# Kernel tuning notes

Measured on AMD Instinct MI355X. Metric: run time of the kernel, lower is better.

## Reference

```python
import jax, jax.numpy as jnp
import numpy as np

LEVELS = [5023, 1256, 314, 79, 20]  # mesh vertex counts, fine -> coarse
T = 64        # number of audio frames
LATENT = 128  # latent_channels
S = 9         # spiral length
OUT_CH = [32, 64, 64, 128]


def setup_inputs() -> dict:
    key = jax.random.key(0)
    ks = list(jax.random.split(key, 40))
    nk = lambda: ks.pop()
    inp = {}
    inp["latent"] = jax.random.normal(nk(), (T, LATENT), jnp.float32)
    inp["actor"] = jax.random.normal(nk(), (LEVELS[0], 3), jnp.float32)
    # spiral indices per mesh level (levels 0..3 carry SpiralConvs)
    for l in range(4):
        n = LEVELS[l]
        inp[f"spiral{l}"] = jax.random.randint(nk(), (n, S), 0, n)
    # sparse up-transforms: level l+1 (coarse) -> level l (fine), ~3 nnz per fine vertex
    for l in range(4):
        nf, nc = LEVELS[l], LEVELS[l + 1]
        nnz = 3 * nf
        inp[f"up{l}_rows"] = jax.random.randint(nk(), (nnz,), 0, nf)
        inp[f"up{l}_cols"] = jax.random.randint(nk(), (nnz,), 0, nc)
        inp[f"up{l}_vals"] = jax.random.uniform(nk(), (nnz,), jnp.float32)
    def lin(k, od, idim):
        scale = np.sqrt(2.0 / (od + idim)).astype(np.float32)  # xavier-uniform-ish std
        return jax.random.normal(k, (od, idim), jnp.float32) * scale
    # de_layers[0]: Linear(latent -> num_vert * out_channels[-1])
    inp["W0"] = lin(nk(), LEVELS[4] * OUT_CH[-1], LATENT)
    inp["b0"] = jnp.zeros((LEVELS[4] * OUT_CH[-1],), jnp.float32)
    # SpiralDeblock convs (coarse -> fine): 128->128, 128->64, 64->64, 64->32
    inp["W1"] = lin(nk(), 128, 128 * S); inp["b1"] = jnp.zeros((128,), jnp.float32)
    inp["W2"] = lin(nk(), 64, 128 * S);  inp["b2"] = jnp.zeros((64,), jnp.float32)
    inp["W3"] = lin(nk(), 64, 64 * S);   inp["b3"] = jnp.zeros((64,), jnp.float32)
    inp["W4"] = lin(nk(), 32, 64 * S);   inp["b4"] = jnp.zeros((32,), jnp.float32)
    # final SpiralConv 32 -> 3 (init=True in torch zeros it; use small randn for testing)
    inp["Wf"] = lin(nk(), 3, 32 * S) * 0.1
    inp["bf"] = jnp.zeros((3,), jnp.float32)
    return inp


def spiral_conv(x, idx, W, b):
    # x: [T, n_in, C]; idx: [n, S] -> gather spiral neighborhoods, flatten, linear
    t, n = x.shape[0], idx.shape[0]
    g = x[:, idx.reshape(-1), :].reshape(t, n, -1)  # [T, n, S*C]
    return g @ W.T + b


def pool(x, rows, cols, vals, n_out):
    # sparse up-transform: out[:, rows] += x[:, cols] * vals  (scatter-add)
    g = x[:, cols, :] * vals[None, :, None]  # [T, nnz, C]
    return jnp.zeros((x.shape[0], n_out, x.shape[2]), x.dtype).at[:, rows].add(g)


def reference(latent, actor, spiral0, spiral1, spiral2, spiral3,
              up0_rows, up0_cols, up0_vals, up1_rows, up1_cols, up1_vals,
              up2_rows, up2_cols, up2_vals, up3_rows, up3_cols, up3_vals,
              W0, b0, W1, b1, W2, b2, W3, b3, W4, b4, Wf, bf):
    t = latent.shape[0]
    x = (latent @ W0.T + b0).reshape(t, LEVELS[4], OUT_CH[-1])  # [T, 20, 128]
    x = jax.nn.elu(spiral_conv(pool(x, up3_rows, up3_cols, up3_vals, LEVELS[3]), spiral3, W1, b1))
    x = jax.nn.elu(spiral_conv(pool(x, up2_rows, up2_cols, up2_vals, LEVELS[2]), spiral2, W2, b2))
    x = jax.nn.elu(spiral_conv(pool(x, up1_rows, up1_cols, up1_vals, LEVELS[1]), spiral1, W3, b3))
    x = jax.nn.elu(spiral_conv(pool(x, up0_rows, up0_cols, up0_vals, LEVELS[0]), spiral0, W4, b4))
    x = spiral_conv(x, spiral0, Wf, bf)  # [T, 5023, 3]
    return x + actor[None]  # per-frame offsets added to neutral actor mesh
```

## Files before the change

kernel.cpp:

```cpp
#include <hip/hip_runtime.h>
#include <hip/hip_bf16.h>

#define T_FRAMES 64

typedef __bf16 bf16x8 __attribute__((ext_vector_type(8)));
typedef float f32x4 __attribute__((ext_vector_type(4)));

#define NNZ0 15069
#define NNZ1 3768
#define NNZ2 942
#define NNZ3 237
#define N0 5023
#define N1 1256
#define N2 314
#define N3 79
#define N4 20


__global__ __launch_bounds__(256) void linear0_kernel(
    const float* __restrict__ latent, const float* __restrict__ W0,
    const float* __restrict__ b0, __bf16* __restrict__ out) {
  int id = blockIdx.x * 256 + threadIdx.x;
  if (id >= 64 * 2560) return;
  int j = id % 2560;
  int t = id / 2560;
  const float* lrow = latent + t * 128;
  const float* wrow = W0 + j * 128;
  float acc = b0[j];
#pragma unroll 8
  for (int k = 0; k < 128; ++k) acc = fmaf(lrow[k], wrow[k], acc);
  out[((size_t)(j >> 7) * 64 + t) * 128 + (j & 127)] = (__bf16)acc;
}

__global__ __launch_bounds__(256) void cvt_all_kernel(
    const float* __restrict__ W1, const float* __restrict__ W2,
    const float* __restrict__ W3, const float* __restrict__ W4,
    const float* __restrict__ Wf, __bf16* __restrict__ o) {
  int i = blockIdx.x * 256 + threadIdx.x;
  if (i < 147456) { o[i] = (__bf16)W1[i]; return; }
  if (i < 221184) { o[i] = (__bf16)W2[i - 147456]; return; }
  if (i < 258048) { o[i] = (__bf16)W3[i - 221184]; return; }
  if (i < 276480) { o[i] = (__bf16)W4[i - 258048]; return; }
  if (i < 281088) {
    int j = i - 276480;
    o[i] = (j / 288 < 3) ? (__bf16)Wf[j] : (__bf16)0.f;
  }
}

__global__ __launch_bounds__(256) void csr_count_kernel(
    const int* __restrict__ r0, const int* __restrict__ r1,
    const int* __restrict__ r2, const int* __restrict__ r3,
    int* __restrict__ c0, int* __restrict__ c1,
    int* __restrict__ c2, int* __restrict__ c3) {
  int i = blockIdx.x * 256 + threadIdx.x;
  if (i < NNZ0) atomicAdd(&c0[r0[i]], 1);
  else if (i < NNZ0 + NNZ1) atomicAdd(&c1[r1[i - NNZ0]], 1);
  else if (i < NNZ0 + NNZ1 + NNZ2) atomicAdd(&c2[r2[i - NNZ0 - NNZ1]], 1);
  else if (i < NNZ0 + NNZ1 + NNZ2 + NNZ3) atomicAdd(&c3[r3[i - NNZ0 - NNZ1 - NNZ2]], 1);
}

__global__ __launch_bounds__(256) void csr_scan_kernel(
    const int* __restrict__ c0, const int* __restrict__ c1,
    const int* __restrict__ c2, const int* __restrict__ c3,
    int* __restrict__ o0, int* __restrict__ o1,
    int* __restrict__ o2, int* __restrict__ o3,
    int* __restrict__ u0, int* __restrict__ u1,
    int* __restrict__ u2, int* __restrict__ u3) {
  const int b = blockIdx.x;
  const int* counts = b == 0 ? c0 : b == 1 ? c1 : b == 2 ? c2 : c3;
  int* off = b == 0 ? o0 : b == 1 ? o1 : b == 2 ? o2 : o3;
  int* cur = b == 0 ? u0 : b == 1 ? u1 : b == 2 ? u2 : u3;
  const int n = b == 0 ? N0 : b == 1 ? N1 : b == 2 ? N2 : N3;

  __shared__ int part[256];
  const int chunk = (n + 255) / 256;
  const int start = threadIdx.x * chunk;
  const int end = min(start + chunk, n);
  int s = 0;
  for (int i = start; i < end; ++i) s += counts[i];
  part[threadIdx.x] = s;
  __syncthreads();
  for (int d = 1; d < 256; d <<= 1) {
    int v = (threadIdx.x >= d) ? part[threadIdx.x - d] : 0;
    __syncthreads();
    part[threadIdx.x] += v;
    __syncthreads();
  }
  int run = (threadIdx.x == 0) ? 0 : part[threadIdx.x - 1];
  for (int i = start; i < end; ++i) {
    off[i] = run;
    cur[i] = run;
    run += counts[i];
  }
  if (threadIdx.x == 255) off[n] = run;
}

__global__ __launch_bounds__(256) void csr_bucket_kernel(
    const int* __restrict__ r0, const int* __restrict__ r1,
    const int* __restrict__ r2, const int* __restrict__ r3,
    const int* __restrict__ q0, const int* __restrict__ q1,
    const int* __restrict__ q2, const int* __restrict__ q3,
    const float* __restrict__ v0, const float* __restrict__ v1,
    const float* __restrict__ v2, const float* __restrict__ v3,
    int* __restrict__ u0, int* __restrict__ u1,
    int* __restrict__ u2, int* __restrict__ u3,
    int2* __restrict__ p0, int2* __restrict__ p1,
    int2* __restrict__ p2, int2* __restrict__ p3) {
  int i = blockIdx.x * 256 + threadIdx.x;
  if (i < NNZ0) {
    int p = atomicAdd(&u0[r0[i]], 1);
    p0[p] = make_int2(q0[i], __float_as_int(v0[i]));
  } else if (i < NNZ0 + NNZ1) {
    int e = i - NNZ0;
    int p = atomicAdd(&u1[r1[e]], 1);
    p1[p] = make_int2(q1[e], __float_as_int(v1[e]));
  } else if (i < NNZ0 + NNZ1 + NNZ2) {
    int e = i - NNZ0 - NNZ1;
    int p = atomicAdd(&u2[r2[e]], 1);
    p2[p] = make_int2(q2[e], __float_as_int(v2[e]));
  } else if (i < NNZ0 + NNZ1 + NNZ2 + NNZ3) {
    int e = i - NNZ0 - NNZ1 - NNZ2;
    int p = atomicAdd(&u3[r3[e]], 1);
    p3[p] = make_int2(q3[e], __float_as_int(v3[e]));
  }
}

template <int C, int TT>
__global__ __launch_bounds__(256) void pool_csr_kernel(
    const __bf16* __restrict__ x, const int* __restrict__ off,
    const int2* __restrict__ pk, __bf16* __restrict__ out, int n_out) {
  unsigned id = blockIdx.x * 256u + threadIdx.x;
  unsigned total = (unsigned)n_out * (T_FRAMES / TT) * C;
  if (id >= total) return;
  const int c = id % C;
  const unsigned rt = id / C;
  const int tb = rt % (T_FRAMES / TT);
  const int row = rt / (T_FRAMES / TT);

  const int o0 = off[row], o1 = off[row + 1];
  float acc[TT];
#pragma unroll
  for (int u = 0; u < TT; ++u) acc[u] = 0.f;

  for (int j = o0; j < o1; ++j) {
    const int2 rec = pk[j];
    const float val = __int_as_float(rec.y);
    const __bf16* xp = x + ((size_t)rec.x * T_FRAMES + tb * TT) * C + c;
#pragma unroll
    for (int u = 0; u < TT; ++u)
      acc[u] = fmaf(val, (float)xp[(size_t)u * C], acc[u]);
  }

  __bf16* op = out + ((size_t)row * T_FRAMES + tb * TT) * C + c;
#pragma unroll
  for (int u = 0; u < TT; ++u) op[(size_t)u * C] = (__bf16)acc[u];
}

template <int CIN, int COUT, int WV, int MT>
__global__ __launch_bounds__(256) void conv_mfma_kernel(
    const __bf16* __restrict__ x, const int* __restrict__ idx,
    const __bf16* __restrict__ Wb, const float* __restrict__ bias,
    __bf16* __restrict__ out) {
  constexpr int K = 9 * CIN;
  constexpr int KK = K / 32;
  constexpr int NT = COUT / 16;

  const int lane = threadIdx.x & 63;
  const int wid = threadIdx.x >> 6;
  const int v = blockIdx.x;
  const int tq0 = (blockIdx.y * WV + wid) * MT;
  const int col = lane & 15;
  const int kg = lane >> 4;

  size_t vbase[9];
#pragma unroll
  for (int s = 0; s < 9; ++s)
    vbase[s] = (size_t)idx[v * 9 + s] * (T_FRAMES * CIN);

  bf16x8 a[MT][KK];
#pragma unroll
  for (int mt = 0; mt < MT; ++mt) {
    const size_t trow = (size_t)(tq0 + mt) * 16 + col;
#pragma unroll
    for (int kk = 0; kk < KK; ++kk) {
      const int s = (kk * 32) / CIN;
      const int ci0 = (kk * 32) % CIN;
      a[mt][kk] = *(const bf16x8*)(x + vbase[s] + trow * CIN + ci0 + kg * 8);
    }
  }

  f32x4 acc[MT][NT];
#pragma unroll
  for (int nt = 0; nt < NT; ++nt) {
    float b = bias[nt * 16 + col];
#pragma unroll
    for (int mt = 0; mt < MT; ++mt) acc[mt][nt] = (f32x4){b, b, b, b};
  }

#pragma unroll
  for (int kk = 0; kk < KK; ++kk) {
#pragma unroll
    for (int nt = 0; nt < NT; ++nt) {
      bf16x8 bfr = *(const bf16x8*)(Wb + (size_t)(nt * 16 + col) * K + kk * 32 + kg * 8);
#pragma unroll
      for (int mt = 0; mt < MT; ++mt)
        acc[mt][nt] = __builtin_amdgcn_mfma_f32_16x16x32_bf16(a[mt][kk], bfr, acc[mt][nt], 0, 0, 0);
    }
  }

#pragma unroll
  for (int mt = 0; mt < MT; ++mt) {
#pragma unroll
    for (int j = 0; j < 4; ++j) {
      const size_t tr = (size_t)(tq0 + mt) * 16 + kg * 4 + j;
#pragma unroll
      for (int nt = 0; nt < NT; ++nt) {
        float aa = acc[mt][nt][j];
        aa = aa > 0.f ? aa : expm1f(aa);
        out[((size_t)v * T_FRAMES + tr) * COUT + nt * 16 + col] = (__bf16)aa;
      }
    }
  }
}

__global__ __launch_bounds__(256) void final_mfma_kernel(
    const __bf16* __restrict__ x, const int* __restrict__ idx,
    const __bf16* __restrict__ Wfp, const float* __restrict__ bf3,
    const float* __restrict__ actor, float* __restrict__ out) {
  const int lane = threadIdx.x & 63;
  const int wid = threadIdx.x >> 6;
  const int v = blockIdx.x;
  const int col = lane & 15;
  const int kg = lane >> 4;
  const size_t trow = (size_t)wid * 16 + col;

  bf16x8 a[9];
#pragma unroll
  for (int s = 0; s < 9; ++s)
    a[s] = *(const bf16x8*)(x + (size_t)idx[v * 9 + s] * (T_FRAMES * 32) + trow * 32 + kg * 8);

  float b = (col < 3) ? bf3[col] : 0.f;
  f32x4 acc = (f32x4){b, b, b, b};

#pragma unroll
  for (int kk = 0; kk < 9; ++kk) {
    bf16x8 w = *(const bf16x8*)(Wfp + col * 288 + kk * 32 + kg * 8);
    acc = __builtin_amdgcn_mfma_f32_16x16x32_bf16(a[kk], w, acc, 0, 0, 0);
  }

  if (col < 3) {
    const float av = actor[v * 3 + col];
#pragma unroll
    for (int j = 0; j < 4; ++j) {
      const int tr = wid * 16 + kg * 4 + j;
      out[((size_t)tr * N0 + v) * 3 + col] = acc[j] + av;
    }
  }
}

extern "C" void kernel_launch(void* const* d_in, const int* in_sizes, int n_in_args,
                              void* d_out, int out_size, void* d_ws, size_t ws_size,
                              hipStream_t stream) {
  const float* latent = (const float*)d_in[0];
  const float* actor  = (const float*)d_in[1];
  const int* spiral0 = (const int*)d_in[2];
  const int* spiral1 = (const int*)d_in[3];
  const int* spiral2 = (const int*)d_in[4];
  const int* spiral3 = (const int*)d_in[5];
  const int* up0_rows = (const int*)d_in[6];
  const int* up0_cols = (const int*)d_in[7];
  const float* up0_vals = (const float*)d_in[8];
  const int* up1_rows = (const int*)d_in[9];
  const int* up1_cols = (const int*)d_in[10];
  const float* up1_vals = (const float*)d_in[11];
  const int* up2_rows = (const int*)d_in[12];
  const int* up2_cols = (const int*)d_in[13];
  const float* up2_vals = (const float*)d_in[14];
  const int* up3_rows = (const int*)d_in[15];
  const int* up3_cols = (const int*)d_in[16];
  const float* up3_vals = (const float*)d_in[17];
  const float* W0 = (const float*)d_in[18];
  const float* b0 = (const float*)d_in[19];
  const float* W1 = (const float*)d_in[20];
  const float* b1 = (const float*)d_in[21];
  const float* W2 = (const float*)d_in[22];
  const float* b2 = (const float*)d_in[23];
  const float* W3 = (const float*)d_in[24];
  const float* b3 = (const float*)d_in[25];
  const float* W4 = (const float*)d_in[26];
  const float* b4 = (const float*)d_in[27];
  const float* Wf = (const float*)d_in[28];
  const float* bf3 = (const float*)d_in[29];
  float* out = (float*)d_out;

  __bf16* poolbuf = (__bf16*)d_ws;
  __bf16* convout = poolbuf + 20574208;
  __bf16* wbuf = convout + 10287104;
  __bf16* W1b = wbuf;
  __bf16* W2b = W1b + 147456;
  __bf16* W3b = W2b + 73728;
  __bf16* W4b = W3b + 36864;
  __bf16* Wfp = W4b + 18432;
  int* csr = (int*)(wbuf + 281088);
  int* cnt0 = csr;            int* cnt1 = cnt0 + N0;   int* cnt2 = cnt1 + N1;   int* cnt3 = cnt2 + N2;
  int* off0 = csr + 6672;     int* off1 = off0 + N0+1; int* off2 = off1 + N1+1; int* off3 = off2 + N2+1;
  int* cur0 = csr + 13348;    int* cur1 = cur0 + N0;   int* cur2 = cur1 + N1;   int* cur3 = cur2 + N2;
  int2* pk0 = (int2*)(csr + 20020);
  int2* pk1 = pk0 + NNZ0;
  int2* pk2 = pk1 + NNZ1;
  int2* pk3 = pk2 + NNZ2;

  hipMemsetAsync(cnt0, 0, 6672 * sizeof(int), stream);
  csr_count_kernel<<<(20016 + 255) / 256, 256, 0, stream>>>(
      up0_rows, up1_rows, up2_rows, up3_rows, cnt0, cnt1, cnt2, cnt3);
  csr_scan_kernel<<<4, 256, 0, stream>>>(cnt0, cnt1, cnt2, cnt3,
                                         off0, off1, off2, off3,
                                         cur0, cur1, cur2, cur3);
  csr_bucket_kernel<<<(20016 + 255) / 256, 256, 0, stream>>>(
      up0_rows, up1_rows, up2_rows, up3_rows,
      up0_cols, up1_cols, up2_cols, up3_cols,
      up0_vals, up1_vals, up2_vals, up3_vals,
      cur0, cur1, cur2, cur3, pk0, pk1, pk2, pk3);

  cvt_all_kernel<<<(281088 + 255) / 256, 256, 0, stream>>>(W1, W2, W3, W4, Wf, wbuf);

  linear0_kernel<<<(64 * 2560 + 255) / 256, 256, 0, stream>>>(latent, W0, b0, convout);

  pool_csr_kernel<128, 16><<<(N3 * 4 * 128 + 255) / 256, 256, 0, stream>>>(
      convout, off3, pk3, poolbuf, N3);
  conv_mfma_kernel<128, 128, 1, 1><<<dim3(N3, 4), 64, 0, stream>>>(
      poolbuf, spiral3, W1b, b1, convout);

  pool_csr_kernel<128, 16><<<(N2 * 4 * 128 + 255) / 256, 256, 0, stream>>>(
      convout, off2, pk2, poolbuf, N2);
  conv_mfma_kernel<128, 64, 1, 1><<<dim3(N2, 4), 64, 0, stream>>>(
      poolbuf, spiral2, W2b, b2, convout);

  pool_csr_kernel<64, 16><<<(N1 * 4 * 64 + 255) / 256, 256, 0, stream>>>(
      convout, off1, pk1, poolbuf, N1);
  conv_mfma_kernel<64, 64, 2, 2><<<dim3(N1, 1), 128, 0, stream>>>(
      poolbuf, spiral1, W3b, b3, convout);

  pool_csr_kernel<64, 16><<<(N0 * 4 * 64 + 255) / 256, 256, 0, stream>>>(
      convout, off0, pk0, poolbuf, N0);
  conv_mfma_kernel<64, 32, 2, 2><<<dim3(N0, 1), 128, 0, stream>>>(
      poolbuf, spiral0, W4b, b4, convout);

  final_mfma_kernel<<<N0, 256, 0, stream>>>(convout, spiral0, Wfp, bf3, actor, out);
}
```

Baseline: 406.2 us.

## Reorder final spiral conv: project per vertex first, then gather-sum projections

Splits the final 32->3 spiral convolution into a dense per-vertex MFMA projection against each of the 9 spiral weight slices, followed by a gather kernel that sums the projected 3-channel values over spiral neighbours and adds bias and actor. This cuts the gathered data per output vertex from 32 channels to 4. In exchange it adds a kernel launch, a temporary buffer written and re-read, and bf16 rounding of partial sums. Launch bounds for the conv kernel are also tightened to match the actual block size.

```diff
diff --git a/kernel.cpp b/kernel.cpp
--- a/kernel.cpp
+++ b/kernel.cpp
@@ -4,6 +4,7 @@
 #define T_FRAMES 64
 
 typedef __bf16 bf16x8 __attribute__((ext_vector_type(8)));
+typedef __bf16 bf16x4 __attribute__((ext_vector_type(4)));
 typedef float f32x4 __attribute__((ext_vector_type(4)));
 
 #define NNZ0 15069
@@ -157,7 +158,7 @@
 }
 
 template <int CIN, int COUT, int WV, int MT>
-__global__ __launch_bounds__(256) void conv_mfma_kernel(
+__global__ __launch_bounds__(WV * 64) void conv_mfma_kernel(
     const __bf16* __restrict__ x, const int* __restrict__ idx,
     const __bf16* __restrict__ Wb, const float* __restrict__ bias,
     __bf16* __restrict__ out) {
@@ -223,39 +224,55 @@
   }
 }
 
-__global__ __launch_bounds__(256) void final_mfma_kernel(
-    const __bf16* __restrict__ x, const int* __restrict__ idx,
-    const __bf16* __restrict__ Wfp, const float* __restrict__ bf3,
-    const float* __restrict__ actor, float* __restrict__ out) {
+__global__ __launch_bounds__(256) void final_dense_kernel(
+    const __bf16* __restrict__ z, const __bf16* __restrict__ Wfp,
+    __bf16* __restrict__ Z) {
   const int lane = threadIdx.x & 63;
   const int wid = threadIdx.x >> 6;
-  const int v = blockIdx.x;
+  const int u = blockIdx.x;
   const int col = lane & 15;
   const int kg = lane >> 4;
   const size_t trow = (size_t)wid * 16 + col;
 
-  bf16x8 a[9];
-#pragma unroll
-  for (int s = 0; s < 9; ++s)
-    a[s] = *(const bf16x8*)(x + (size_t)idx[v * 9 + s] * (T_FRAMES * 32) + trow * 32 + kg * 8);
-
-  float b = (col < 3) ? bf3[col] : 0.f;
-  f32x4 acc = (f32x4){b, b, b, b};
-
-#pragma unroll
-  for (int kk = 0; kk < 9; ++kk) {
-    bf16x8 w = *(const bf16x8*)(Wfp + col * 288 + kk * 32 + kg * 8);
-    acc = __builtin_amdgcn_mfma_f32_16x16x32_bf16(a[kk], w, acc, 0, 0, 0);
-  }
-
-  if (col < 3) {
-    const float av = actor[v * 3 + col];
-#pragma unroll
-    for (int j = 0; j < 4; ++j) {
-      const int tr = wid * 16 + kg * 4 + j;
-      out[((size_t)tr * N0 + v) * 3 + col] = acc[j] + av;
+  const bf16x8 a = *(const bf16x8*)(z + ((size_t)u * T_FRAMES + trow) * 32 + kg * 8);
+
+#pragma unroll
+  for (int s = 0; s < 9; ++s) {
+    const bf16x8 w = *(const bf16x8*)(Wfp + col * 288 + s * 32 + kg * 8);
+    f32x4 acc = (f32x4){0.f, 0.f, 0.f, 0.f};
+    acc = __builtin_amdgcn_mfma_f32_16x16x32_bf16(a, w, acc, 0, 0, 0);
+    if (col < 4) {
+#pragma unroll
+      for (int j = 0; j < 4; ++j) {
+        const size_t tr = (size_t)wid * 16 + kg * 4 + j;
+        Z[(((size_t)u * 9 + s) * T_FRAMES + tr) * 4 + col] = (__bf16)acc[j];
+      }
     }
   }
+}
+
+__global__ __launch_bounds__(256) void final_gather_kernel(
+    const __bf16* __restrict__ Z, const int* __restrict__ idx,
+    const float* __restrict__ bf3, const float* __restrict__ actor,
+    float* __restrict__ out) {
+  const unsigned id = blockIdx.x * 256u + threadIdx.x;
+  if (id >= (unsigned)N0 * T_FRAMES) return;
+  const int t = id & 63;
+  const int v = id >> 6;
+
+  float a0 = bf3[0], a1 = bf3[1], a2 = bf3[2];
+#pragma unroll
+  for (int s = 0; s < 9; ++s) {
+    const int u = idx[v * 9 + s];
+    const bf16x4 zz = *(const bf16x4*)(Z + (((size_t)u * 9 + s) * T_FRAMES + t) * 4);
+    a0 += (float)zz[0];
+    a1 += (float)zz[1];
+    a2 += (float)zz[2];
+  }
+  float* op = out + ((size_t)t * N0 + v) * 3;
+  op[0] = a0 + actor[v * 3 + 0];
+  op[1] = a1 + actor[v * 3 + 1];
+  op[2] = a2 + actor[v * 3 + 2];
 }
 
 extern "C" void kernel_launch(void* const* d_in, const int* in_sizes, int n_in_args,
@@ -309,6 +326,7 @@
   int2* pk1 = pk0 + NNZ0;
   int2* pk2 = pk1 + NNZ1;
   int2* pk3 = pk2 + NNZ2;
+  __bf16* Zbuf = poolbuf;
 
   hipMemsetAsync(cnt0, 0, 6672 * sizeof(int), stream);
   csr_count_kernel<<<(20016 + 255) / 256, 256, 0, stream>>>(
@@ -346,5 +364,7 @@
   conv_mfma_kernel<64, 32, 2, 2><<<dim3(N0, 1), 128, 0, stream>>>(
       poolbuf, spiral0, W4b, b4, convout);
 
-  final_mfma_kernel<<<N0, 256, 0, stream>>>(convout, spiral0, Wfp, bf3, actor, out);
-}
+  final_dense_kernel<<<N0, 256, 0, stream>>>(convout, Wfp, Zbuf);
+  final_gather_kernel<<<(N0 * T_FRAMES + 255) / 256, 256, 0, stream>>>(
+      Zbuf, spiral0, bf3, actor, out);
+}
```

Measured after the change: 407.3 us. No clear change (+0.3%).
